# Performance work log

Measured on AMD Instinct MI355X. Metric: run time of the kernel, lower is better.

Reference implementation:

```python
import jax, jax.numpy as jnp
import numpy as np

B, T, D, U, OUT = 64, 1024, 512, 512, 4

def setup_inputs() -> dict:
    key = jax.random.key(0)
    ks = jax.random.split(key, 6)
    s = lambda n: 1.0 / np.sqrt(n)
    return {
        "tx": jax.random.normal(ks[0], (B, T, D), dtype=jnp.float32),
        "kernel": jax.random.normal(ks[1], (D, 4 * U), dtype=jnp.float32) * s(D),
        "recurrent_kernel": jax.random.normal(ks[2], (U, 4 * U), dtype=jnp.float32) * s(U),
        "bias": jnp.zeros((4 * U,), dtype=jnp.float32),
        "fc_w": jax.random.normal(ks[3], (U, OUT), dtype=jnp.float32) * s(U),
        "fc_b": jnp.zeros((OUT,), dtype=jnp.float32),
    }

def reference(tx, kernel, recurrent_kernel, bias, fc_w, fc_b):
    b, t, d = tx.shape
    u = recurrent_kernel.shape[0]
    # Fuse the 4 per-gate input matmuls into one GEMM over all timesteps: [B,T,4U]
    xz = jnp.einsum('btd,dk->btk', tx, kernel) + bias

    def step(carry, xz_t):
        h, c = carry
        z = xz_t + h @ recurrent_kernel  # fused 4 recurrent matmuls
        z1, z2, z3, z4 = jnp.split(z, 4, axis=-1)
        v1 = jnp.tanh(z1)
        v2 = jax.nn.sigmoid(z2)
        v3 = jax.nn.sigmoid(z3)
        v4 = jax.nn.sigmoid(z4)
        c = v1 * v2 + v3 * c
        h = v4 * jnp.tanh(c)
        return (h, c), None

    h0 = jnp.zeros((b, u), dtype=tx.dtype)
    c0 = jnp.zeros((b, u), dtype=tx.dtype)
    (h_last, _), _ = jax.lax.scan(step, (h0, c0), jnp.swapaxes(xz, 0, 1))
    # RNN(return_sequences=False) -> last hidden state, then Dense + softmax
    return jax.nn.softmax(h_last @ fc_w + fc_b, axis=-1)
```

## Files before the change

kernel.cpp:

```cpp
#include <hip/hip_runtime.h>
#include <stdint.h>

typedef short sv8 __attribute__((ext_vector_type(8)));
typedef float fv4 __attribute__((ext_vector_type(4)));
typedef uint32_t u32x4 __attribute__((ext_vector_type(4)));
typedef uint32_t u32x2 __attribute__((ext_vector_type(2)));

__device__ __forceinline__ uint16_t f2bf(float f) {
    uint32_t u = __builtin_bit_cast(uint32_t, f);
    u += 0x7FFFu + ((u >> 16) & 1u);
    return (uint16_t)(u >> 16);
}
__device__ __forceinline__ float bf2f(uint16_t h) {
    uint32_t u = ((uint32_t)h) << 16;
    return __builtin_bit_cast(float, u);
}
__device__ __forceinline__ void split4(float4 f, ushort4& h, ushort4& l) {
    h.x = f2bf(f.x); l.x = f2bf(f.x - bf2f(h.x));
    h.y = f2bf(f.y); l.y = f2bf(f.y - bf2f(h.y));
    h.z = f2bf(f.z); l.z = f2bf(f.z - bf2f(h.z));
    h.w = f2bf(f.w); l.w = f2bf(f.w - bf2f(h.w));
}
__device__ __forceinline__ float fsig(float x)  { return 1.f / (1.f + __expf(-x)); }
__device__ __forceinline__ float ftanh(float x) { return 1.f - 2.f / (__expf(2.f * x) + 1.f); }

__device__ __forceinline__ u32x4 load16_cc(const void* p) {
    u32x4 r;
    asm volatile("global_load_dwordx4 %0, %1, off sc0 sc1" : "=v"(r) : "v"(p) : "memory");
    return r;
}
__device__ __forceinline__ uint32_t load4_cc(const void* p) {
    uint32_t r;
    asm volatile("global_load_dword %0, %1, off sc0 sc1" : "=v"(r) : "v"(p) : "memory");
    return r;
}
__device__ __forceinline__ void atom8_st(void* p, u32x2 v) {
    asm volatile("global_atomic_swap_x2 %0, %1, off" :: "v"(p), "v"(v) : "memory");
}
__device__ __forceinline__ void atom4_st(void* p, uint32_t v) {
    asm volatile("global_atomic_swap %0, %1, off" :: "v"(p), "v"(v) : "memory");
}

#define TT     1024
#define DD     512
#define NN     2048
#define TCH    128
#define NCHUNK 8
#define NREG   8
#define RSTRIDE 16

__global__ void prep_split_b(const float* __restrict__ kern,
                             uint16_t* __restrict__ bth, uint16_t* __restrict__ btl) {
    int tid = blockIdx.x * 256 + threadIdx.x;
    if (tid >= DD * NN) return;
    int k = tid >> 11;
    int n = tid & (NN - 1);
    float v = kern[tid];
    uint16_t h = f2bf(v);
    bth[n * DD + k] = h;
    btl[n * DD + k] = f2bf(v - bf2f(h));
}

__global__ void prep_rk(const float* __restrict__ rk,
                        uint16_t* __restrict__ rkh, uint16_t* __restrict__ rkl) {
    int tid = blockIdx.x * 256 + threadIdx.x;
    if (tid >= 128 * 16 * 64 * 8) return;
    int j = tid & 7, lane = (tid >> 3) & 63, kt = (tid >> 9) & 15, g = tid >> 13;
    int lq = lane >> 4, c = lane & 15;
    int k = kt * 32 + lq * 8 + j;
    int colg = (c >> 2) * 512 + g * 4 + (c & 3);
    float v = rk[(size_t)k * NN + colg];
    uint16_t h = f2bf(v);
    rkh[tid] = h;
    rkl[tid] = f2bf(v - bf2f(h));
}

__global__ __launch_bounds__(256, 2) void gemm_xz(
    const float* __restrict__ tx, int t0,
    const uint16_t* __restrict__ Bth, const uint16_t* __restrict__ Btl,
    float* __restrict__ xz) {
    __shared__ __align__(16) uint16_t sA[2][128 * 32];
    __shared__ __align__(16) uint16_t sB[2][128 * 32];
    int tid = threadIdx.x, lane = tid & 63, w = tid >> 6;
    int btile = blockIdx.x >> 4;
    int n0 = (blockIdx.x & 15) * 128;
    int wm = (w >> 1) * 64, wn = (w & 1) * 64;
    int srow = tid >> 1, scol = (tid & 1) * 16;

    fv4 acc[4][4];
#pragma unroll
    for (int q = 0; q < 4; q++)
#pragma unroll
        for (int r = 0; r < 4; r++) acc[q][r] = (fv4){0.f, 0.f, 0.f, 0.f};

    const float* abase = tx + ((size_t)btile * TT + t0 + srow) * DD + scol;

    for (int k0 = 0; k0 < DD; k0 += 32) {
        const float4* A4 = (const float4*)(abase + k0);
        float4 f0 = A4[0], f1 = A4[1], f2 = A4[2], f3 = A4[3];
        const uint16_t* pb  = Bth + (size_t)(n0 + srow) * DD + k0 + scol;
        const uint16_t* pbl = Btl + (size_t)(n0 + srow) * DD + k0 + scol;
        uint4 b0 = *(const uint4*)pb,  b1 = *(const uint4*)(pb + 8);
        uint4 c0 = *(const uint4*)pbl, c1 = *(const uint4*)(pbl + 8);
        union { ushort4 v4[4]; uint4 q[2]; } H, L;
        split4(f0, H.v4[0], L.v4[0]);
        split4(f1, H.v4[1], L.v4[1]);
        split4(f2, H.v4[2], L.v4[2]);
        split4(f3, H.v4[3], L.v4[3]);
        __syncthreads();
        *(uint4*)&sA[0][srow * 32 + scol]     = H.q[0];
        *(uint4*)&sA[0][srow * 32 + scol + 8] = H.q[1];
        *(uint4*)&sA[1][srow * 32 + scol]     = L.q[0];
        *(uint4*)&sA[1][srow * 32 + scol + 8] = L.q[1];
        *(uint4*)&sB[0][srow * 32 + scol]     = b0;
        *(uint4*)&sB[0][srow * 32 + scol + 8] = b1;
        *(uint4*)&sB[1][srow * 32 + scol]     = c0;
        *(uint4*)&sB[1][srow * 32 + scol + 8] = c1;
        __syncthreads();
        sv8 ah[4], al[4], bh[4], bl[4];
#pragma unroll
        for (int q = 0; q < 4; q++) {
            int ra = (wm + q * 16 + (lane & 15)) * 32 + (lane >> 4) * 8;
            ah[q] = *(const sv8*)&sA[0][ra];
            al[q] = *(const sv8*)&sA[1][ra];
        }
#pragma unroll
        for (int r = 0; r < 4; r++) {
            int rb = (wn + r * 16 + (lane & 15)) * 32 + (lane >> 4) * 8;
            bh[r] = *(const sv8*)&sB[0][rb];
            bl[r] = *(const sv8*)&sB[1][rb];
        }
#pragma unroll
        for (int q = 0; q < 4; q++)
#pragma unroll
            for (int r = 0; r < 4; r++) {
                acc[q][r] = __builtin_amdgcn_mfma_f32_16x16x32_bf16(ah[q], bh[r], acc[q][r], 0, 0, 0);
                acc[q][r] = __builtin_amdgcn_mfma_f32_16x16x32_bf16(ah[q], bl[r], acc[q][r], 0, 0, 0);
                acc[q][r] = __builtin_amdgcn_mfma_f32_16x16x32_bf16(al[q], bh[r], acc[q][r], 0, 0, 0);
            }
    }
#pragma unroll
    for (int q = 0; q < 4; q++)
#pragma unroll
        for (int r = 0; r < 4; r++) {
            int tl0 = wm + q * 16 + ((lane >> 4) * 4);
            int ncol = n0 + wn + r * 16 + (lane & 15);
            int gate = ncol >> 9, uu = ncol & 511;
            int cil = gate * 4 + (uu & 3);
            int g = uu >> 2;
#pragma unroll
            for (int e = 0; e < 4; e++) {
                size_t idx = (((size_t)(g * 64 + btile) * TCH + (tl0 + e)) << 4) + cil;
                xz[idx] = acc[q][r][e];
            }
        }
}

__global__ __launch_bounds__(512, 1) void lstm_rec(
    const uint16_t* __restrict__ rkh, const uint16_t* __restrict__ rkl,
    const float* __restrict__ bias, const float* __restrict__ xz,
    char* __restrict__ hbuf, uint32_t* __restrict__ rdy,
    float* __restrict__ cstate, float* __restrict__ hlast, int gbase) {
    __shared__ __align__(16) uint16_t ls[32768];
    int wg = blockIdx.x, tid = threadIdx.x;
    int lane = tid & 63, w = tid >> 6;
    int wb = w >> 1, ct = w & 1;
    int c = lane & 15, lq = lane >> 4;
    int u = wg * 8 + ct * 4 + (c & 3);
    int g = u >> 2;
    int colg = (c >> 2) * 512 + u;

    sv8 BH[16], BL[16];
    {
        const sv8* ph = (const sv8*)rkh + (size_t)g * 1024 + lane;
        const sv8* pl = (const sv8*)rkl + (size_t)g * 1024 + lane;
#pragma unroll
        for (int kt = 0; kt < 16; kt++) {
            BH[kt] = ph[kt * 64];
            BL[kt] = pl[kt * 64];
        }
    }
    float bv = bias[colg];
    int b0 = wb * 16 + lq * 4;
    float cst[4];
#pragma unroll
    for (int r = 0; r < 4; r++) cst[r] = cstate[(b0 + r) * 512 + u];
    const float* xzb = xz + ((size_t)(g * 64 + b0) * TCH) * 16 + c;
    int off_w_short = ((wb * 16 + (wg >> 2)) * 64 + lq * 4 + 16 * (wg & 3)) * 8 + ct * 4;
    int own = (lane == wg) ? 1 : 0;

    for (int tl = 0; tl < TCH; tl++) {
        int t = gbase + tl;
        const float* xzt = xzb + tl * 16;
        float xzv[4];
#pragma unroll
        for (int r = 0; r < 4; r++) xzv[r] = xzt[r * (TCH * 16)];

        {
            const uint32_t* rp = rdy + (size_t)((t & (NREG - 1)) * 64 + lane) * RSTRIDE;
            uint32_t want = (uint32_t)t;
            for (;;) {
                uint32_t v = load4_cc(rp);
                asm volatile("s_waitcnt vmcnt(0)" ::: "memory");
                if (__all(own | (int)(v >= want))) break;
            }
        }
        const char* src = hbuf + (size_t)(t & (NREG - 1)) * 65536 + tid * 16;
        u32x4 hv[8];
#pragma unroll
        for (int i = 0; i < 8; i++) hv[i] = load16_cc(src + i * 8192);
        asm volatile("s_waitcnt vmcnt(0)" ::: "memory");
        __builtin_amdgcn_sched_barrier(0);
#pragma unroll
        for (int i = 0; i < 8; i++) *(u32x4*)&ls[i * 4096 + tid * 8] = hv[i];
        __syncthreads();

        fv4 aH = (fv4){0.f, 0.f, 0.f, 0.f};
        fv4 aL = (fv4){0.f, 0.f, 0.f, 0.f};
#pragma unroll
        for (int half = 0; half < 2; half++) {
            sv8 af[8];
#pragma unroll
            for (int k8 = 0; k8 < 8; k8++)
                af[k8] = *(const sv8*)&ls[((wb * 16 + half * 8 + k8) * 64 + lane) * 8];
#pragma unroll
            for (int k8 = 0; k8 < 8; k8++) {
                aH = __builtin_amdgcn_mfma_f32_16x16x32_bf16(af[k8], BH[half * 8 + k8], aH, 0, 0, 0);
                aL = __builtin_amdgcn_mfma_f32_16x16x32_bf16(af[k8], BL[half * 8 + k8], aL, 0, 0, 0);
            }
        }

        char* wdst = hbuf + (size_t)((t + 1) & (NREG - 1)) * 65536;
#pragma unroll
        for (int r = 0; r < 4; r++) {
            float z  = aH[r] + aL[r] + bv + xzv[r];
            float z2 = __shfl_xor(z, 4);
            float z3 = __shfl_xor(z, 8);
            float z4 = __shfl_xor(z, 12);
            float v1 = ftanh(z);
            float v2 = fsig(z2);
            float v3 = fsig(z3);
            float v4 = fsig(z4);
            cst[r] = v1 * v2 + v3 * cst[r];
            float hn = v4 * ftanh(cst[r]);
            uint32_t hbts = (uint32_t)f2bf(hn);
            int bsl = lane & 48;
            uint32_t h0 = __shfl(hbts, bsl);
            uint32_t h1 = __shfl(hbts, bsl + 1);
            uint32_t h2 = __shfl(hbts, bsl + 2);
            uint32_t h3 = __shfl(hbts, bsl + 3);
            if (c == 0) {
                u32x2 pk = (u32x2){h0 | (h1 << 16), h2 | (h3 << 16)};
                atom8_st(wdst + (size_t)(off_w_short + r * 8) * 2, pk);
            }
            if (t == TT - 1 && c < 4) hlast[(b0 + r) * 512 + u] = hn;
        }
        asm volatile("s_waitcnt vmcnt(0)" ::: "memory");
        __syncthreads();
        if (tid == 0)
            atom4_st(rdy + (size_t)(((t + 1) & (NREG - 1)) * 64 + wg) * RSTRIDE,
                     (uint32_t)(t + 1));
    }
    if (c < 4) {
#pragma unroll
        for (int r = 0; r < 4; r++) cstate[(b0 + r) * 512 + u] = cst[r];
    }
    asm volatile("s_waitcnt vmcnt(0)" ::: "memory");
}

__global__ void final_out(const float* __restrict__ hlast, const float* __restrict__ fcw,
                          const float* __restrict__ fcb, float* __restrict__ out) {
    __shared__ float lg[256];
    int tid = threadIdx.x;
    int b = tid >> 2, o = tid & 3;
    float s = fcb[o];
    const float* hr = hlast + b * 512;
    for (int k = 0; k < 512; k++) s += hr[k] * fcw[k * 4 + o];
    lg[tid] = s;
    __syncthreads();
    float l0 = lg[b * 4 + 0], l1 = lg[b * 4 + 1], l2 = lg[b * 4 + 2], l3 = lg[b * 4 + 3];
    float m = fmaxf(fmaxf(l0, l1), fmaxf(l2, l3));
    float sum = expf(l0 - m) + expf(l1 - m) + expf(l2 - m) + expf(l3 - m);
    out[tid] = expf(s - m) / sum;
}

extern "C" void kernel_launch(void* const* d_in, const int* in_sizes, int n_in,
                              void* d_out, int out_size, void* d_ws, size_t ws_size,
                              hipStream_t stream) {
    const float* tx   = (const float*)d_in[0];
    const float* kern = (const float*)d_in[1];
    const float* rk   = (const float*)d_in[2];
    const float* bias = (const float*)d_in[3];
    const float* fcw  = (const float*)d_in[4];
    const float* fcb  = (const float*)d_in[5];
    float* out = (float*)d_out;

    char* ws = (char*)d_ws;
    size_t off = 0;
    auto alloc = [&](size_t bytes) -> void* {
        void* p = ws + off;
        off += (bytes + 255) & ~(size_t)255;
        return p;
    };
    float*    xzc    = (float*)alloc((size_t)128 * 64 * TCH * 16 * 4);
    uint16_t* Bth    = (uint16_t*)alloc((size_t)NN * DD * 2);
    uint16_t* Btl    = (uint16_t*)alloc((size_t)NN * DD * 2);
    uint16_t* rkh    = (uint16_t*)alloc((size_t)128 * 16 * 64 * 8 * 2);
    uint16_t* rkl    = (uint16_t*)alloc((size_t)128 * 16 * 64 * 8 * 2);
    char*     hbuf   = (char*)alloc((size_t)NREG * 65536);
    uint32_t* rdy    = (uint32_t*)alloc((size_t)NREG * 64 * RSTRIDE * 4);
    float*    cstate = (float*)alloc(64 * 512 * 4);
    float*    hlast  = (float*)alloc(64 * 512 * 4);

    hipMemsetAsync(hbuf, 0, 65536, stream);
    hipMemsetAsync(rdy, 0, (size_t)NREG * 64 * RSTRIDE * 4, stream);
    hipMemsetAsync(cstate, 0, 64 * 512 * 4, stream);

    prep_split_b<<<4096, 256, 0, stream>>>(kern, Bth, Btl);
    prep_rk<<<4096, 256, 0, stream>>>(rk, rkh, rkl);

    for (int chunk = 0; chunk < NCHUNK; ++chunk) {
        gemm_xz<<<1024, 256, 0, stream>>>(tx, chunk * TCH, Bth, Btl, xzc);
        lstm_rec<<<64, 512, 0, stream>>>(rkh, rkl, bias, xzc, hbuf, rdy,
                                         cstate, hlast, chunk * TCH);
    }
    final_out<<<1, 256, 0, stream>>>(hlast, fcw, fcb, out);
}
```

Baseline: 5.469 ms.

## Replace ready-flag barrier with NaN-sentinel polling on hidden-state buffer

Removes the per-step ready-flag array. Each block now polls the hidden-state ring buffer itself until no bf16 word equals a quiet-NaN sentinel, and it re-poisons the slot from two steps earlier after consuming it. LDS is double-buffered so the trailing syncthreads, the store wait and the flag write can be dropped. This removes one round trip of flag publish and poll per timestep, at the cost of polling the full payload. It relies on real h values never encoding as 0x7FC0 and on the ordering of the poison writes.

```diff
diff --git a/kernel.cpp b/kernel.cpp
--- a/kernel.cpp
+++ b/kernel.cpp
@@ -29,16 +29,8 @@
     asm volatile("global_load_dwordx4 %0, %1, off sc0 sc1" : "=v"(r) : "v"(p) : "memory");
     return r;
 }
-__device__ __forceinline__ uint32_t load4_cc(const void* p) {
-    uint32_t r;
-    asm volatile("global_load_dword %0, %1, off sc0 sc1" : "=v"(r) : "v"(p) : "memory");
-    return r;
-}
 __device__ __forceinline__ void atom8_st(void* p, u32x2 v) {
     asm volatile("global_atomic_swap_x2 %0, %1, off" :: "v"(p), "v"(v) : "memory");
-}
-__device__ __forceinline__ void atom4_st(void* p, uint32_t v) {
-    asm volatile("global_atomic_swap %0, %1, off" :: "v"(p), "v"(v) : "memory");
 }
 
 #define TT     1024
@@ -47,7 +39,7 @@
 #define TCH    128
 #define NCHUNK 8
 #define NREG   8
-#define RSTRIDE 16
+#define SENTW  0x7FC07FC0u
 
 __global__ void prep_split_b(const float* __restrict__ kern,
                              uint16_t* __restrict__ bth, uint16_t* __restrict__ btl) {
@@ -73,6 +65,12 @@
     uint16_t h = f2bf(v);
     rkh[tid] = h;
     rkl[tid] = f2bf(v - bf2f(h));
+}
+
+__global__ void prep_poison(uint32_t* __restrict__ hbuf) {
+    int tid = blockIdx.x * 256 + threadIdx.x;
+    if (tid >= 7 * 16384) return;
+    hbuf[16384 + tid] = SENTW;
 }
 
 __global__ __launch_bounds__(256, 2) void gemm_xz(
@@ -159,9 +157,9 @@
 __global__ __launch_bounds__(512, 1) void lstm_rec(
     const uint16_t* __restrict__ rkh, const uint16_t* __restrict__ rkl,
     const float* __restrict__ bias, const float* __restrict__ xz,
-    char* __restrict__ hbuf, uint32_t* __restrict__ rdy,
-    float* __restrict__ cstate, float* __restrict__ hlast, int gbase) {
-    __shared__ __align__(16) uint16_t ls[32768];
+    char* __restrict__ hbuf, float* __restrict__ cstate,
+    float* __restrict__ hlast, int gbase) {
+    __shared__ __align__(16) uint16_t ls[2][32768];
     int wg = blockIdx.x, tid = threadIdx.x;
     int lane = tid & 63, w = tid >> 6;
     int wb = w >> 1, ct = w & 1;
@@ -187,33 +185,50 @@
     for (int r = 0; r < 4; r++) cst[r] = cstate[(b0 + r) * 512 + u];
     const float* xzb = xz + ((size_t)(g * 64 + b0) * TCH) * 16 + c;
     int off_w_short = ((wb * 16 + (wg >> 2)) * 64 + lq * 4 + 16 * (wg & 3)) * 8 + ct * 4;
-    int own = (lane == wg) ? 1 : 0;
+    const u32x2 sent2 = (u32x2){SENTW, SENTW};
 
     for (int tl = 0; tl < TCH; tl++) {
         int t = gbase + tl;
+        int buf = t & 1;
         const float* xzt = xzb + tl * 16;
         float xzv[4];
 #pragma unroll
         for (int r = 0; r < 4; r++) xzv[r] = xzt[r * (TCH * 16)];
 
         {
-            const uint32_t* rp = rdy + (size_t)((t & (NREG - 1)) * 64 + lane) * RSTRIDE;
-            uint32_t want = (uint32_t)t;
-            for (;;) {
-                uint32_t v = load4_cc(rp);
+            const char* src = hbuf + (size_t)(t & (NREG - 1)) * 65536 + tid * 16;
+            uint32_t mask = 0xFFu;
+            do {
+                u32x4 tmp[8];
+#pragma unroll
+                for (int i = 0; i < 8; i++)
+                    if (mask & (1u << i)) tmp[i] = load16_cc(src + i * 8192);
                 asm volatile("s_waitcnt vmcnt(0)" ::: "memory");
-                if (__all(own | (int)(v >= want))) break;
-            }
-        }
-        const char* src = hbuf + (size_t)(t & (NREG - 1)) * 65536 + tid * 16;
-        u32x4 hv[8];
-#pragma unroll
-        for (int i = 0; i < 8; i++) hv[i] = load16_cc(src + i * 8192);
-        asm volatile("s_waitcnt vmcnt(0)" ::: "memory");
-        __builtin_amdgcn_sched_barrier(0);
-#pragma unroll
-        for (int i = 0; i < 8; i++) *(u32x4*)&ls[i * 4096 + tid * 8] = hv[i];
+                __builtin_amdgcn_sched_barrier(0);
+#pragma unroll
+                for (int i = 0; i < 8; i++) {
+                    if (mask & (1u << i)) {
+                        uint32_t bad = 0;
+#pragma unroll
+                        for (int q = 0; q < 4; q++) {
+                            uint32_t word = tmp[i][q];
+                            bad |= (uint32_t)(((word & 0xFFFFu) == 0x7FC0u) |
+                                              ((word >> 16) == 0x7FC0u));
+                        }
+                        if (!bad) {
+                            *(u32x4*)&ls[buf][i * 4096 + tid * 8] = tmp[i];
+                            mask &= ~(1u << i);
+                        }
+                    }
+                }
+            } while (mask);
+        }
         __syncthreads();
+
+        if (tid < 128) {
+            char* pz = hbuf + (size_t)((t - 1) & (NREG - 1)) * 65536 + wg * 1024 + tid * 8;
+            atom8_st(pz, sent2);
+        }
 
         fv4 aH = (fv4){0.f, 0.f, 0.f, 0.f};
         fv4 aL = (fv4){0.f, 0.f, 0.f, 0.f};
@@ -222,7 +237,7 @@
             sv8 af[8];
 #pragma unroll
             for (int k8 = 0; k8 < 8; k8++)
-                af[k8] = *(const sv8*)&ls[((wb * 16 + half * 8 + k8) * 64 + lane) * 8];
+                af[k8] = *(const sv8*)&ls[buf][((wb * 16 + half * 8 + k8) * 64 + lane) * 8];
 #pragma unroll
             for (int k8 = 0; k8 < 8; k8++) {
                 aH = __builtin_amdgcn_mfma_f32_16x16x32_bf16(af[k8], BH[half * 8 + k8], aH, 0, 0, 0);
@@ -255,11 +270,6 @@
             }
             if (t == TT - 1 && c < 4) hlast[(b0 + r) * 512 + u] = hn;
         }
-        asm volatile("s_waitcnt vmcnt(0)" ::: "memory");
-        __syncthreads();
-        if (tid == 0)
-            atom4_st(rdy + (size_t)(((t + 1) & (NREG - 1)) * 64 + wg) * RSTRIDE,
-                     (uint32_t)(t + 1));
     }
     if (c < 4) {
 #pragma unroll
@@ -308,20 +318,19 @@
     uint16_t* rkh    = (uint16_t*)alloc((size_t)128 * 16 * 64 * 8 * 2);
     uint16_t* rkl    = (uint16_t*)alloc((size_t)128 * 16 * 64 * 8 * 2);
     char*     hbuf   = (char*)alloc((size_t)NREG * 65536);
-    uint32_t* rdy    = (uint32_t*)alloc((size_t)NREG * 64 * RSTRIDE * 4);
     float*    cstate = (float*)alloc(64 * 512 * 4);
     float*    hlast  = (float*)alloc(64 * 512 * 4);
 
     hipMemsetAsync(hbuf, 0, 65536, stream);
-    hipMemsetAsync(rdy, 0, (size_t)NREG * 64 * RSTRIDE * 4, stream);
     hipMemsetAsync(cstate, 0, 64 * 512 * 4, stream);
 
     prep_split_b<<<4096, 256, 0, stream>>>(kern, Bth, Btl);
     prep_rk<<<4096, 256, 0, stream>>>(rk, rkh, rkl);
+    prep_poison<<<448, 256, 0, stream>>>((uint32_t*)hbuf);
 
     for (int chunk = 0; chunk < NCHUNK; ++chunk) {
         gemm_xz<<<1024, 256, 0, stream>>>(tx, chunk * TCH, Bth, Btl, xzc);
-        lstm_rec<<<64, 512, 0, stream>>>(rkh, rkl, bias, xzc, hbuf, rdy,
+        lstm_rec<<<64, 512, 0, stream>>>(rkh, rkl, bias, xzc, hbuf,
                                          cstate, hlast, chunk * TCH);
     }
     final_out<<<1, 256, 0, stream>>>(hlast, fcw, fcb, out);
```

Result: slower. 6.217 ms (+13.7%).

## Overlap next chunk's input GEMM with current chunk's recurrence in one launch

Applied to the files above, without the earlier changes.

Adds a fused kernel in which the first 64 blocks run the LSTM recurrence for the current time chunk while the other 192 blocks compute the input projection for the next chunk into a second xz buffer. The GEMM work is spread over these blocks, each holding two 256-thread sub-tiles. This hides the input GEMM behind the latency-bound recurrence on otherwise idle CUs. The cost is a second xz workspace buffer, a fallback path when the workspace is too small, and possible memory and cache contention slowing the recurrence's cross-block spin synchronisation.

```diff
diff --git a/kernel.cpp b/kernel.cpp
--- a/kernel.cpp
+++ b/kernel.cpp
@@ -75,94 +75,105 @@
     rkl[tid] = f2bf(v - bf2f(h));
 }
 
+__device__ __forceinline__ void gemm_tile(
+    const float* __restrict__ tx, int t0,
+    const uint16_t* __restrict__ Bth, const uint16_t* __restrict__ Btl,
+    float* __restrict__ xz, uint16_t* sb, int t256, int btile, int n0, int act) {
+    int lane = t256 & 63, w = t256 >> 6;
+    int wm = (w >> 1) * 64, wn = (w & 1) * 64;
+    int srow = t256 >> 1, scol = (t256 & 1) * 16;
+    fv4 acc[4][4];
+#pragma unroll
+    for (int q = 0; q < 4; q++)
+#pragma unroll
+        for (int r = 0; r < 4; r++) acc[q][r] = (fv4){0.f, 0.f, 0.f, 0.f};
+
+    const float* abase = tx + ((size_t)btile * TT + t0 + srow) * DD + scol;
+
+    for (int k0 = 0; k0 < DD; k0 += 32) {
+        float4 f0, f1, f2, f3;
+        uint4 b0, b1, c0, c1;
+        if (act) {
+            const float4* A4 = (const float4*)(abase + k0);
+            f0 = A4[0]; f1 = A4[1]; f2 = A4[2]; f3 = A4[3];
+            const uint16_t* pb  = Bth + (size_t)(n0 + srow) * DD + k0 + scol;
+            const uint16_t* pbl = Btl + (size_t)(n0 + srow) * DD + k0 + scol;
+            b0 = *(const uint4*)pb;  b1 = *(const uint4*)(pb + 8);
+            c0 = *(const uint4*)pbl; c1 = *(const uint4*)(pbl + 8);
+        }
+        __syncthreads();
+        if (act) {
+            union { ushort4 v4[4]; uint4 q[2]; } H, L;
+            split4(f0, H.v4[0], L.v4[0]);
+            split4(f1, H.v4[1], L.v4[1]);
+            split4(f2, H.v4[2], L.v4[2]);
+            split4(f3, H.v4[3], L.v4[3]);
+            *(uint4*)&sb[srow * 32 + scol]            = H.q[0];
+            *(uint4*)&sb[srow * 32 + scol + 8]        = H.q[1];
+            *(uint4*)&sb[4096 + srow * 32 + scol]     = L.q[0];
+            *(uint4*)&sb[4096 + srow * 32 + scol + 8] = L.q[1];
+            *(uint4*)&sb[8192 + srow * 32 + scol]     = b0;
+            *(uint4*)&sb[8192 + srow * 32 + scol + 8] = b1;
+            *(uint4*)&sb[12288 + srow * 32 + scol]    = c0;
+            *(uint4*)&sb[12288 + srow * 32 + scol + 8]= c1;
+        }
+        __syncthreads();
+        sv8 ah[4], al[4], bh[4], bl[4];
+#pragma unroll
+        for (int q = 0; q < 4; q++) {
+            int ra = (wm + q * 16 + (lane & 15)) * 32 + (lane >> 4) * 8;
+            ah[q] = *(const sv8*)&sb[ra];
+            al[q] = *(const sv8*)&sb[4096 + ra];
+        }
+#pragma unroll
+        for (int r = 0; r < 4; r++) {
+            int rb = (wn + r * 16 + (lane & 15)) * 32 + (lane >> 4) * 8;
+            bh[r] = *(const sv8*)&sb[8192 + rb];
+            bl[r] = *(const sv8*)&sb[12288 + rb];
+        }
+#pragma unroll
+        for (int q = 0; q < 4; q++)
+#pragma unroll
+            for (int r = 0; r < 4; r++) {
+                acc[q][r] = __builtin_amdgcn_mfma_f32_16x16x32_bf16(ah[q], bh[r], acc[q][r], 0, 0, 0);
+                acc[q][r] = __builtin_amdgcn_mfma_f32_16x16x32_bf16(ah[q], bl[r], acc[q][r], 0, 0, 0);
+                acc[q][r] = __builtin_amdgcn_mfma_f32_16x16x32_bf16(al[q], bh[r], acc[q][r], 0, 0, 0);
+            }
+    }
+    if (act) {
+#pragma unroll
+        for (int q = 0; q < 4; q++)
+#pragma unroll
+            for (int r = 0; r < 4; r++) {
+                int tl0 = wm + q * 16 + ((lane >> 4) * 4);
+                int ncol = n0 + wn + r * 16 + (lane & 15);
+                int gate = ncol >> 9, uu = ncol & 511;
+                int cil = gate * 4 + (uu & 3);
+                int g = uu >> 2;
+#pragma unroll
+                for (int e = 0; e < 4; e++) {
+                    size_t idx = (((size_t)(g * 64 + btile) * TCH + (tl0 + e)) << 4) + cil;
+                    xz[idx] = acc[q][r][e];
+                }
+            }
+    }
+}
+
 __global__ __launch_bounds__(256, 2) void gemm_xz(
     const float* __restrict__ tx, int t0,
     const uint16_t* __restrict__ Bth, const uint16_t* __restrict__ Btl,
     float* __restrict__ xz) {
-    __shared__ __align__(16) uint16_t sA[2][128 * 32];
-    __shared__ __align__(16) uint16_t sB[2][128 * 32];
-    int tid = threadIdx.x, lane = tid & 63, w = tid >> 6;
-    int btile = blockIdx.x >> 4;
-    int n0 = (blockIdx.x & 15) * 128;
-    int wm = (w >> 1) * 64, wn = (w & 1) * 64;
-    int srow = tid >> 1, scol = (tid & 1) * 16;
-
-    fv4 acc[4][4];
-#pragma unroll
-    for (int q = 0; q < 4; q++)
-#pragma unroll
-        for (int r = 0; r < 4; r++) acc[q][r] = (fv4){0.f, 0.f, 0.f, 0.f};
-
-    const float* abase = tx + ((size_t)btile * TT + t0 + srow) * DD + scol;
-
-    for (int k0 = 0; k0 < DD; k0 += 32) {
-        const float4* A4 = (const float4*)(abase + k0);
-        float4 f0 = A4[0], f1 = A4[1], f2 = A4[2], f3 = A4[3];
-        const uint16_t* pb  = Bth + (size_t)(n0 + srow) * DD + k0 + scol;
-        const uint16_t* pbl = Btl + (size_t)(n0 + srow) * DD + k0 + scol;
-        uint4 b0 = *(const uint4*)pb,  b1 = *(const uint4*)(pb + 8);
-        uint4 c0 = *(const uint4*)pbl, c1 = *(const uint4*)(pbl + 8);
-        union { ushort4 v4[4]; uint4 q[2]; } H, L;
-        split4(f0, H.v4[0], L.v4[0]);
-        split4(f1, H.v4[1], L.v4[1]);
-        split4(f2, H.v4[2], L.v4[2]);
-        split4(f3, H.v4[3], L.v4[3]);
-        __syncthreads();
-        *(uint4*)&sA[0][srow * 32 + scol]     = H.q[0];
-        *(uint4*)&sA[0][srow * 32 + scol + 8] = H.q[1];
-        *(uint4*)&sA[1][srow * 32 + scol]     = L.q[0];
-        *(uint4*)&sA[1][srow * 32 + scol + 8] = L.q[1];
-        *(uint4*)&sB[0][srow * 32 + scol]     = b0;
-        *(uint4*)&sB[0][srow * 32 + scol + 8] = b1;
-        *(uint4*)&sB[1][srow * 32 + scol]     = c0;
-        *(uint4*)&sB[1][srow * 32 + scol + 8] = c1;
-        __syncthreads();
-        sv8 ah[4], al[4], bh[4], bl[4];
-#pragma unroll
-        for (int q = 0; q < 4; q++) {
-            int ra = (wm + q * 16 + (lane & 15)) * 32 + (lane >> 4) * 8;
-            ah[q] = *(const sv8*)&sA[0][ra];
-            al[q] = *(const sv8*)&sA[1][ra];
-        }
-#pragma unroll
-        for (int r = 0; r < 4; r++) {
-            int rb = (wn + r * 16 + (lane & 15)) * 32 + (lane >> 4) * 8;
-            bh[r] = *(const sv8*)&sB[0][rb];
-            bl[r] = *(const sv8*)&sB[1][rb];
-        }
-#pragma unroll
-        for (int q = 0; q < 4; q++)
-#pragma unroll
-            for (int r = 0; r < 4; r++) {
-                acc[q][r] = __builtin_amdgcn_mfma_f32_16x16x32_bf16(ah[q], bh[r], acc[q][r], 0, 0, 0);
-                acc[q][r] = __builtin_amdgcn_mfma_f32_16x16x32_bf16(ah[q], bl[r], acc[q][r], 0, 0, 0);
-                acc[q][r] = __builtin_amdgcn_mfma_f32_16x16x32_bf16(al[q], bh[r], acc[q][r], 0, 0, 0);
-            }
-    }
-#pragma unroll
-    for (int q = 0; q < 4; q++)
-#pragma unroll
-        for (int r = 0; r < 4; r++) {
-            int tl0 = wm + q * 16 + ((lane >> 4) * 4);
-            int ncol = n0 + wn + r * 16 + (lane & 15);
-            int gate = ncol >> 9, uu = ncol & 511;
-            int cil = gate * 4 + (uu & 3);
-            int g = uu >> 2;
-#pragma unroll
-            for (int e = 0; e < 4; e++) {
-                size_t idx = (((size_t)(g * 64 + btile) * TCH + (tl0 + e)) << 4) + cil;
-                xz[idx] = acc[q][r][e];
-            }
-        }
-}
-
-__global__ __launch_bounds__(512, 1) void lstm_rec(
+    __shared__ __align__(16) uint16_t sb[16384];
+    gemm_tile(tx, t0, Bth, Btl, xz, sb, threadIdx.x,
+              blockIdx.x >> 4, (blockIdx.x & 15) * 128, 1);
+}
+
+__device__ __forceinline__ void lstm_body(
     const uint16_t* __restrict__ rkh, const uint16_t* __restrict__ rkl,
     const float* __restrict__ bias, const float* __restrict__ xz,
     char* __restrict__ hbuf, uint32_t* __restrict__ rdy,
-    float* __restrict__ cstate, float* __restrict__ hlast, int gbase) {
-    __shared__ __align__(16) uint16_t ls[32768];
-    int wg = blockIdx.x, tid = threadIdx.x;
+    float* __restrict__ cstate, float* __restrict__ hlast, int gbase,
+    uint16_t* ls , int wg, int tid) {
     int lane = tid & 63, w = tid >> 6;
     int wb = w >> 1, ct = w & 1;
     int c = lane & 15, lq = lane >> 4;
@@ -268,6 +279,45 @@
     asm volatile("s_waitcnt vmcnt(0)" ::: "memory");
 }
 
+__global__ __launch_bounds__(512, 1) void lstm_rec(
+    const uint16_t* __restrict__ rkh, const uint16_t* __restrict__ rkl,
+    const float* __restrict__ bias, const float* __restrict__ xz,
+    char* __restrict__ hbuf, uint32_t* __restrict__ rdy,
+    float* __restrict__ cstate, float* __restrict__ hlast, int gbase) {
+    __shared__ __align__(16) uint16_t ls[32768];
+    lstm_body(rkh, rkl, bias, xz, hbuf, rdy, cstate, hlast, gbase,
+              ls, blockIdx.x, threadIdx.x);
+}
+
+__global__ __launch_bounds__(512, 1) void fused_step(
+    const uint16_t* __restrict__ rkh, const uint16_t* __restrict__ rkl,
+    const float* __restrict__ bias, const float* __restrict__ xz_cur,
+    char* __restrict__ hbuf, uint32_t* __restrict__ rdy,
+    float* __restrict__ cstate, float* __restrict__ hlast, int gbase,
+    const float* __restrict__ tx, int t0_next,
+    const uint16_t* __restrict__ Bth, const uint16_t* __restrict__ Btl,
+    float* __restrict__ xz_next) {
+    __shared__ __align__(16) uint16_t shm[32768];
+    int bid = blockIdx.x, tid = threadIdx.x;
+    if (bid < 64) {
+        lstm_body(rkh, rkl, bias, xz_cur, hbuf, rdy, cstate, hlast, gbase,
+                  shm, bid, tid);
+    } else {
+        if (t0_next < 0) return;
+        int t256 = tid & 255, subwg = tid >> 8;
+        uint16_t* sb = shm + subwg * 16384;
+        int slot = (bid - 64) * 2 + subwg;
+#pragma unroll 1
+        for (int it = 0; it < 3; ++it) {
+            int tile = slot + it * 384;
+            int act = tile < 1024;
+            int btile = (tile < 1024 ? tile : 0) >> 4;
+            int n0 = ((tile < 1024 ? tile : 0) & 15) * 128;
+            gemm_tile(tx, t0_next, Bth, Btl, xz_next, sb, t256, btile, n0, act);
+        }
+    }
+}
+
 __global__ void final_out(const float* __restrict__ hlast, const float* __restrict__ fcw,
                           const float* __restrict__ fcb, float* __restrict__ out) {
     __shared__ float lg[256];
@@ -302,7 +352,7 @@
         off += (bytes + 255) & ~(size_t)255;
         return p;
     };
-    float*    xzc    = (float*)alloc((size_t)128 * 64 * TCH * 16 * 4);
+    float*    xz0    = (float*)alloc((size_t)128 * 64 * TCH * 16 * 4);
     uint16_t* Bth    = (uint16_t*)alloc((size_t)NN * DD * 2);
     uint16_t* Btl    = (uint16_t*)alloc((size_t)NN * DD * 2);
     uint16_t* rkh    = (uint16_t*)alloc((size_t)128 * 16 * 64 * 8 * 2);
@@ -311,6 +361,11 @@
     uint32_t* rdy    = (uint32_t*)alloc((size_t)NREG * 64 * RSTRIDE * 4);
     float*    cstate = (float*)alloc(64 * 512 * 4);
     float*    hlast  = (float*)alloc(64 * 512 * 4);
+    size_t small_need = off;
+    float*    xz1    = (float*)alloc((size_t)128 * 64 * TCH * 16 * 4);
+    size_t big_need = off;
+    int big = (ws_size >= big_need);
+    if (ws_size < small_need) big = 0;
 
     hipMemsetAsync(hbuf, 0, 65536, stream);
     hipMemsetAsync(rdy, 0, (size_t)NREG * 64 * RSTRIDE * 4, stream);
@@ -319,10 +374,22 @@
     prep_split_b<<<4096, 256, 0, stream>>>(kern, Bth, Btl);
     prep_rk<<<4096, 256, 0, stream>>>(rk, rkh, rkl);
 
-    for (int chunk = 0; chunk < NCHUNK; ++chunk) {
-        gemm_xz<<<1024, 256, 0, stream>>>(tx, chunk * TCH, Bth, Btl, xzc);
-        lstm_rec<<<64, 512, 0, stream>>>(rkh, rkl, bias, xzc, hbuf, rdy,
-                                         cstate, hlast, chunk * TCH);
+    if (big) {
+        gemm_xz<<<1024, 256, 0, stream>>>(tx, 0, Bth, Btl, xz0);
+        for (int k = 0; k < NCHUNK; ++k) {
+            const float* xzc = (k & 1) ? xz1 : xz0;
+            float*       xzn = (k & 1) ? xz0 : xz1;
+            fused_step<<<256, 512, 0, stream>>>(rkh, rkl, bias, xzc, hbuf, rdy,
+                                                cstate, hlast, k * TCH,
+                                                tx, (k < NCHUNK - 1) ? (k + 1) * TCH : -1,
+                                                Bth, Btl, xzn);
+        }
+    } else {
+        for (int k = 0; k < NCHUNK; ++k) {
+            gemm_xz<<<1024, 256, 0, stream>>>(tx, k * TCH, Bth, Btl, xz0);
+            lstm_rec<<<64, 512, 0, stream>>>(rkh, rkl, bias, xz0, hbuf, rdy,
+                                             cstate, hlast, k * TCH);
+        }
     }
     final_out<<<1, 256, 0, stream>>>(hlast, fcw, fcb, out);
 }
```

Measured after the change: 5.086 ms. -7.0%, faster.
